# Optimization experiments

Measured on AMD Instinct MI355X. Metric: run time of the kernel, lower is better.

## Reference

```python
import jax, jax.numpy as jnp
import numpy as np

V = 32000   # vocab / input_size
H = 1024    # hidden_size (== embedding dim)
L = 2       # num_layers
B = 64      # batch
T = 256     # seq_len


def setup_inputs() -> dict:
    key = jax.random.key(0)
    ks = jax.random.split(key, 8)
    s = float(1.0 / np.sqrt(H))  # pytorch default uniform bound for LSTM/Linear
    return {
        "inputs": jax.random.randint(ks[0], (B, T), 0, V),
        "embed_table": jax.random.normal(ks[1], (V, H), jnp.float32),
        "W_ih": jax.random.uniform(ks[2], (L, 4 * H, H), jnp.float32, -s, s),
        "W_hh": jax.random.uniform(ks[3], (L, 4 * H, H), jnp.float32, -s, s),
        "b_ih": jax.random.uniform(ks[4], (L, 4 * H), jnp.float32, -s, s),
        "b_hh": jax.random.uniform(ks[5], (L, 4 * H), jnp.float32, -s, s),
        "W_proj": jax.random.uniform(ks[6], (V, H), jnp.float32, -s, s),
        "b_proj": jnp.zeros((V,), jnp.float32),  # module fills bias with 0
    }


def _lstm_layer(x, Wih, Whh, bih, bhh):
    # x: [B, T, H]. Precompute input contribution for all steps (one big GEMM).
    xg = jnp.einsum("bth,gh->btg", x, Wih) + bih + bhh  # [B, T, 4H]
    h0 = jnp.zeros((x.shape[0], Whh.shape[1]), x.dtype)
    c0 = h0

    def step(carry, xt):
        h, c = carry
        gates = xt + h @ Whh.T  # [B, 4H]
        i, f, g, o = jnp.split(gates, 4, axis=-1)  # pytorch gate order i,f,g,o
        i = jax.nn.sigmoid(i)
        f = jax.nn.sigmoid(f)
        g = jnp.tanh(g)
        o = jax.nn.sigmoid(o)
        c = f * c + i * g
        h = o * jnp.tanh(c)
        return (h, c), h

    (hT, cT), ys = jax.lax.scan(step, (h0, c0), jnp.swapaxes(xg, 0, 1))
    return jnp.swapaxes(ys, 0, 1), hT, cT  # [B,T,H], [B,H], [B,H]


def reference(inputs, embed_table, W_ih, W_hh, b_ih, b_hh, W_proj, b_proj):
    x = embed_table[inputs]  # [B, T, H]
    h_n, c_n = [], []
    for l in range(L):  # small fixed layer loop
        x, hT, cT = _lstm_layer(x, W_ih[l], W_hh[l], b_ih[l], b_hh[l])
        h_n.append(hT)
        c_n.append(cT)
    last_output = x[:, -1]                      # squeeze(output[:, -1]) with B>1 -> [B, H]
    logits = last_output @ W_proj.T + b_proj    # [B, V]
    return last_output, logits, jnp.stack(h_n), jnp.stack(c_n)
```

## Files before the change

### kernel.cpp

```cpp
#include <hip/hip_runtime.h>
#include <hip/hip_bf16.h>
#include <stdint.h>
#include <stddef.h>

typedef __hip_bfloat16 bf16;
typedef __attribute__((ext_vector_type(8))) short bfrag;
typedef __attribute__((ext_vector_type(4))) float ffrag;
typedef unsigned long long u64;

#define HDIM 1024
#define BATCH 64
#define TSTEPS 256
#define GDIM 4096
#define VOCAB 32000

#define HSLOT 16384ull

__device__ __forceinline__ bf16 f2b(float x) { return __float2bfloat16(x); }
__device__ __forceinline__ short f2bs(float x) {
  bf16 b = __float2bfloat16(x);
  return *reinterpret_cast<short*>(&b);
}
__device__ __forceinline__ float bs2f(unsigned short u) {
  union { unsigned int i; float f; } v;
  v.i = ((unsigned int)u) << 16;
  return v.f;
}
__device__ __forceinline__ ffrag mfma16(bfrag a, bfrag b, ffrag c) {
  return __builtin_amdgcn_mfma_f32_16x16x32_bf16(a, b, c, 0, 0, 0);
}
__device__ __forceinline__ float sigm(float x) { return 1.0f / (1.0f + __expf(-x)); }
__device__ __forceinline__ float tanhfast(float x) {
  float e = __expf(2.0f * x);
  return 1.0f - 2.0f / (e + 1.0f);
}

__device__ __forceinline__ void store_u16_agent(unsigned short* p, unsigned short v) {
  __hip_atomic_store(p, v, __ATOMIC_RELAXED, __HIP_MEMORY_SCOPE_AGENT);
}
__device__ __forceinline__ unsigned load_u32_agent(const unsigned* p) {
  return __hip_atomic_load(p, __ATOMIC_RELAXED, __HIP_MEMORY_SCOPE_AGENT);
}
__device__ __forceinline__ void store_u32_agent(unsigned* p, unsigned v) {
  __hip_atomic_store(p, v, __ATOMIC_RELAXED, __HIP_MEMORY_SCOPE_AGENT);
}

__global__ void convert_bf16_kernel(const float* __restrict__ src, bf16* __restrict__ dst, int n4) {
  int i = blockIdx.x * 256 + threadIdx.x;
  if (i >= n4) return;
  float4 v = reinterpret_cast<const float4*>(src)[i];
  ushort4 o;
  o.x = (unsigned short)f2bs(v.x);
  o.y = (unsigned short)f2bs(v.y);
  o.z = (unsigned short)f2bs(v.z);
  o.w = (unsigned short)f2bs(v.w);
  reinterpret_cast<ushort4*>(dst)[i] = o;
}

__global__ void embed_kernel(const int* __restrict__ ids, const float* __restrict__ table,
                             bf16* __restrict__ x, int n4) {
  int i = blockIdx.x * 256 + threadIdx.x;
  if (i >= n4) return;
  int row = i >> 8;
  int c4 = i & 255;
  int tok = ids[row];
  float4 v = reinterpret_cast<const float4*>(table)[(size_t)tok * 256 + c4];
  ushort4 o;
  o.x = (unsigned short)f2bs(v.x);
  o.y = (unsigned short)f2bs(v.y);
  o.z = (unsigned short)f2bs(v.z);
  o.w = (unsigned short)f2bs(v.w);
  reinterpret_cast<ushort4*>(x)[i] = o;
}

#define BMX 128
#define BNX 128
#define BKX 64

template<int LYR>
__launch_bounds__(256, 2)
__global__ void gemm_xg_kernel(const bf16* __restrict__ A,
                               const bf16* __restrict__ W,
                               const float* __restrict__ bih,
                               const float* __restrict__ bhh,
                               bf16* __restrict__ xg) {
  __shared__ bf16 As[BMX][BKX + 8];
  __shared__ bf16 Bs[BNX][BKX + 8];
  const int n0 = blockIdx.x * BNX;
  const int m0 = blockIdx.y * BMX;
  const int tid = threadIdx.x;
  const int w = tid >> 6, l = tid & 63;
  const int wm = (w >> 1) * 64, wn = (w & 1) * 64;
  const int lr = l & 15, lk = (l >> 4) * 8;

  ffrag acc[4][4];
#pragma unroll
  for (int i = 0; i < 4; ++i)
#pragma unroll
    for (int j = 0; j < 4; ++j) acc[i][j] = ffrag{0.f, 0.f, 0.f, 0.f};

  const int sr = tid >> 1, sh = (tid & 1) * 32;
  for (int kb = 0; kb < HDIM; kb += BKX) {
    __syncthreads();
    {
      if (LYR == 0) {
        const uint4* ga = reinterpret_cast<const uint4*>(&A[(size_t)(m0 + sr) * HDIM + kb + sh]);
        uint4* la = reinterpret_cast<uint4*>(&As[sr][sh]);
        la[0] = ga[0]; la[1] = ga[1]; la[2] = ga[2]; la[3] = ga[3];
      } else {
        const u64* hb = (const u64*)A;
        const int m = m0 + sr;
        const size_t tb = (size_t)(255 - (m >> 6)) * HSLOT + (m & 63);
        const int kg0 = (kb + sh) >> 3;
#pragma unroll
        for (int ii = 0; ii < 4; ++ii) {
          u64 lo = hb[tb + (size_t)(kg0 + ii) * 64];
          u64 hi = hb[tb + 8192 + (size_t)(kg0 + ii) * 64];
          *(u64*)&As[sr][sh + ii * 8]     = lo;
          *(u64*)&As[sr][sh + ii * 8 + 4] = hi;
        }
      }
      const uint4* gb = reinterpret_cast<const uint4*>(&W[(size_t)(n0 + sr) * HDIM + kb + sh]);
      uint4* lb = reinterpret_cast<uint4*>(&Bs[sr][sh]);
      lb[0] = gb[0]; lb[1] = gb[1]; lb[2] = gb[2]; lb[3] = gb[3];
    }
    __syncthreads();
#pragma unroll
    for (int ks = 0; ks < 2; ++ks) {
      const int ko = ks * 32 + lk;
      bfrag af[4], bfv[4];
#pragma unroll
      for (int i = 0; i < 4; ++i)
        af[i] = *reinterpret_cast<const bfrag*>(&As[wm + i * 16 + lr][ko]);
#pragma unroll
      for (int j = 0; j < 4; ++j)
        bfv[j] = *reinterpret_cast<const bfrag*>(&Bs[wn + j * 16 + lr][ko]);
#pragma unroll
      for (int i = 0; i < 4; ++i)
#pragma unroll
        for (int j = 0; j < 4; ++j)
          acc[i][j] = mfma16(af[i], bfv[j], acc[i][j]);
    }
  }
  const int rg = (l >> 4) * 4;
#pragma unroll
  for (int j = 0; j < 4; ++j) {
    const int n = n0 + wn + j * 16 + lr;
    const float bias = bih[n] + bhh[n];
    const int q = n >> 10, g = (n & 1023) >> 3, jj = n & 7;
    bf16* base = xg + (size_t)(q * 128 + g) * 16384 * 8 + jj;
#pragma unroll
    for (int i = 0; i < 4; ++i) {
#pragma unroll
      for (int r = 0; r < 4; ++r) {
        const int m = m0 + wm + i * 16 + rg + r;
        base[(size_t)m * 8] = f2b(acc[i][j][r] + bias);
      }
    }
  }
}

__launch_bounds__(256, 1)
__global__ void lstm_seq_kernel(const bf16* __restrict__ xg,
                                const bf16* __restrict__ Whh,
                                bf16* hist,
                                float* __restrict__ out_h,
                                float* __restrict__ out_c,
                                float* __restrict__ out_last,
                                unsigned* __restrict__ flags,
                                int xbs, int xts) {
  __shared__ float gxp[2][16][65];
  const int id = blockIdx.x;
  const int bg = id & 3, cg16 = id >> 2;
  const int tid = threadIdx.x;
  const int w = tid >> 6, l = tid & 63;
  const int lr = l & 15, lkg = l >> 4;
  const int kh = w >> 1, ch = w & 1;
  const int q = lr >> 2, jn = lr & 3;

  bfrag breg0[16], breg1[16];
  {
    const int colbase = cg16 * 16 + ch * 8;
    const size_t r0 = ((size_t)q * HDIM + colbase + jn) * HDIM + kh * 512 + lkg * 8;
    const size_t r1 = ((size_t)q * HDIM + colbase + 4 + jn) * HDIM + kh * 512 + lkg * 8;
#pragma unroll
    for (int ks = 0; ks < 16; ++ks) {
      breg0[ks] = *reinterpret_cast<const bfrag*>(&Whh[r0 + ks * 32]);
      breg1[ks] = *reinterpret_cast<const bfrag*>(&Whh[r1 + ks * 32]);
    }
  }

  const int eb = tid & 15, cl = tid >> 4;
  const int b_glob = bg * 16 + eb;
  const int gpl = cg16 * 2 + (cl >> 3);
  const int xjj = cl & 7;
  const int shalf = (cl >> 2) & 1, sjj = cl & 3;
  float c = 0.0f;

  u64* hb = (u64*)hist;
  const size_t arow = (size_t)(kh * 64 + lkg) * 64 + bg * 16 + lr;
  const unsigned* fv = flags + bg * 64;
  const unsigned short* xgu = (const unsigned short*)xg;

  unsigned short xn[4];
#pragma unroll
  for (int qq = 0; qq < 4; ++qq)
    xn[qq] = xgu[(((size_t)qq * 128 + gpl) * 16384 + (size_t)b_glob * xbs) * 8 + xjj];

#pragma unroll 1
  for (int t = 0; t < TSTEPS; ++t) {
    if (t > 0) {
      const unsigned tt = (unsigned)t;
      for (;;) {
        unsigned f = load_u32_agent(&fv[l]);
        if (__all((int)(f >= tt))) break;
        __builtin_amdgcn_s_sleep(1);
      }
    }
    __builtin_amdgcn_sched_barrier(0);
    asm volatile("" ::: "memory");

    const u64* hin = hb + (size_t)(TSTEPS - t) * HSLOT;
    ffrag a0 = ffrag{0.f, 0.f, 0.f, 0.f};
    ffrag a1 = ffrag{0.f, 0.f, 0.f, 0.f};
#pragma unroll
    for (int ks = 0; ks < 16; ++ks) {
      union { u64 u[2]; bfrag f; } au;
      au.u[0] = hin[arow + ks * 256];
      au.u[1] = hin[8192 + arow + ks * 256];
      a0 = mfma16(au.f, breg0[ks], a0);
      a1 = mfma16(au.f, breg1[ks], a1);
    }
    {
      const int cb = ch * 8;
#pragma unroll
      for (int r = 0; r < 4; ++r) {
        gxp[kh][lkg * 4 + r][q * 16 + cb + jn]     = a0[r];
        gxp[kh][lkg * 4 + r][q * 16 + cb + 4 + jn] = a1[r];
      }
    }
    __syncthreads();

    const float gi = gxp[0][eb][cl]      + gxp[1][eb][cl]      + bs2f(xn[0]);
    const float gf = gxp[0][eb][16 + cl] + gxp[1][eb][16 + cl] + bs2f(xn[1]);
    const float gg = gxp[0][eb][32 + cl] + gxp[1][eb][32 + cl] + bs2f(xn[2]);
    const float go = gxp[0][eb][48 + cl] + gxp[1][eb][48 + cl] + bs2f(xn[3]);
    c = sigm(gf) * c + sigm(gi) * tanhfast(gg);
    const float h = sigm(go) * tanhfast(c);

    u64* hout = hb + (size_t)(255 - t) * HSLOT;
    store_u16_agent((unsigned short*)(hout + (size_t)shalf * 8192 + gpl * 64 + b_glob) + sjj,
                    (unsigned short)f2bs(h));
    if (t == TSTEPS - 1) {
      const int col = cg16 * 16 + cl;
      out_h[(size_t)b_glob * HDIM + col] = h;
      out_c[(size_t)b_glob * HDIM + col] = c;
      if (out_last) out_last[(size_t)b_glob * HDIM + col] = h;
    }
    __builtin_amdgcn_s_waitcnt(0);
    __syncthreads();
    if (t < TSTEPS - 1) {
      if (tid == 0) store_u32_agent(&flags[bg * 64 + cg16], (unsigned)(t + 1));
#pragma unroll
      for (int qq = 0; qq < 4; ++qq)
        xn[qq] = xgu[(((size_t)qq * 128 + gpl) * 16384 +
                      (size_t)b_glob * xbs + (size_t)(t + 1) * xts) * 8 + xjj];
    }
    __builtin_amdgcn_sched_barrier(0);
  }
}

__launch_bounds__(256, 2)
__global__ void logits_kernel(const bf16* __restrict__ hfin,
                              const float* __restrict__ Wp,
                              const float* __restrict__ bp,
                              float* __restrict__ out) {
  const int tid = threadIdx.x;
  const int w = tid >> 6, l = tid & 63;
  const int lr = l & 15, lkg = l >> 4, lk = lkg * 8;
  const int col = blockIdx.x * 64 + w * 16 + lr;
  const float* wrow = &Wp[(size_t)col * HDIM];
  const u64* hb = (const u64*)hfin;
  ffrag acc[4];
#pragma unroll
  for (int i = 0; i < 4; ++i) acc[i] = ffrag{0.f, 0.f, 0.f, 0.f};
#pragma unroll 2
  for (int ks = 0; ks < 32; ++ks) {
    const int k = ks * 32 + lk;
    float4 wa = *reinterpret_cast<const float4*>(&wrow[k]);
    float4 wb = *reinterpret_cast<const float4*>(&wrow[k + 4]);
    bfrag bv;
    bv[0] = f2bs(wa.x); bv[1] = f2bs(wa.y); bv[2] = f2bs(wa.z); bv[3] = f2bs(wa.w);
    bv[4] = f2bs(wb.x); bv[5] = f2bs(wb.y); bv[6] = f2bs(wb.z); bv[7] = f2bs(wb.w);
    const size_t kg = (size_t)(ks * 4 + lkg);
#pragma unroll
    for (int i = 0; i < 4; ++i) {
      union { u64 u[2]; bfrag f; } av;
      av.u[0] = hb[kg * 64 + i * 16 + lr];
      av.u[1] = hb[8192 + kg * 64 + i * 16 + lr];
      acc[i] = mfma16(av.f, bv, acc[i]);
    }
  }
  const float bias = bp[col];
#pragma unroll
  for (int i = 0; i < 4; ++i) {
#pragma unroll
    for (int r = 0; r < 4; ++r) {
      const int b = i * 16 + (l >> 4) * 4 + r;
      out[(size_t)b * VOCAB + col] = acc[i][r] + bias;
    }
  }
}

extern "C" void kernel_launch(void* const* d_in, const int* in_sizes, int n_in,
                              void* d_out, int out_size, void* d_ws, size_t ws_size,
                              hipStream_t stream) {
  const int*   ids   = (const int*)d_in[0];
  const float* table = (const float*)d_in[1];
  const float* Wih   = (const float*)d_in[2];
  const float* Whh   = (const float*)d_in[3];
  const float* bih   = (const float*)d_in[4];
  const float* bhh   = (const float*)d_in[5];
  const float* Wp    = (const float*)d_in[6];
  const float* bp    = (const float*)d_in[7];
  float* out = (float*)d_out;

  char* ws = (char*)d_ws;
  const size_t HISTB_SZ = 257ull * 131072ull;
  const size_t OFF_XG  = 0;
  const size_t OFF_HA  = OFF_XG + (size_t)512 * 16384 * 8 * 2;
  const size_t OFF_HB  = OFF_HA + HISTB_SZ;
  const size_t OFF_WIH = OFF_HB + HISTB_SZ;
  const size_t OFF_WHH = OFF_WIH + (size_t)2 * GDIM * HDIM * 2;
  const size_t OFF_SYNC= OFF_WHH + (size_t)2 * GDIM * HDIM * 2;

  bf16* xg    = (bf16*)(ws + OFF_XG);
  bf16* xb    = (bf16*)(ws + OFF_HA);
  bf16* histA = (bf16*)(ws + OFF_HA);
  bf16* histB = (bf16*)(ws + OFF_HB);
  bf16* wihb  = (bf16*)(ws + OFF_WIH);
  bf16* whhb  = (bf16*)(ws + OFF_WHH);
  unsigned* sync = (unsigned*)(ws + OFF_SYNC);

  (void)hipMemsetAsync(sync, 0, 16384, stream);
  (void)hipMemsetAsync(ws + OFF_HA + 33554432ull, 0, 131072, stream);
  (void)hipMemsetAsync(ws + OFF_HB + 33554432ull, 0, 131072, stream);

  const int nconv4 = 2 * GDIM * HDIM / 4;
  convert_bf16_kernel<<<nconv4 / 256, 256, 0, stream>>>(Wih, wihb, nconv4);
  convert_bf16_kernel<<<nconv4 / 256, 256, 0, stream>>>(Whh, whhb, nconv4);
  const int nemb4 = BATCH * TSTEPS * HDIM / 4;
  embed_kernel<<<nemb4 / 256, 256, 0, stream>>>(ids, table, xb, nemb4);

  float* out_last   = out;
  float* out_logits = out + 65536;
  float* out_hn     = out + 2113536;
  float* out_cn     = out + 2244608;

  gemm_xg_kernel<0><<<dim3(GDIM / BNX, (BATCH * TSTEPS) / BMX), 256, 0, stream>>>(
      xb, wihb, bih, bhh, xg);
  lstm_seq_kernel<<<256, 256, 0, stream>>>(
      xg, whhb, histA, out_hn, out_cn, nullptr, sync, 256, 1);

  gemm_xg_kernel<1><<<dim3(GDIM / BNX, (BATCH * TSTEPS) / BMX), 256, 0, stream>>>(
      histA, wihb + (size_t)GDIM * HDIM, bih + GDIM, bhh + GDIM, xg);
  lstm_seq_kernel<<<256, 256, 0, stream>>>(
      xg, whhb + (size_t)GDIM * HDIM, histB,
      out_hn + (size_t)BATCH * HDIM, out_cn + (size_t)BATCH * HDIM,
      out_last, sync + 256, 1, 64);

  logits_kernel<<<VOCAB / 64, 256, 0, stream>>>(histB, Wp, bp, out_logits);
}
```

Measured before the change: 2.175 ms.

## Overlap layer-2 input GEMM with layer-1 recurrence via flag-gated fused blocks

Layer 1's recurrent kernel is launched with 4096 extra blocks that compute layer 2's input-projection GEMM. Each GEMM tile spin-waits on the layer-1 step flags until its two timesteps of hidden state exist, then computes that tile. The layer-0 GEMM now reads embeddings in time-major order, so the gate buffer is time-major for both layers. Flag polling is also done by one wave followed by a block barrier. The aim is to hide the separate layer-2 GEMM launch behind the serial recurrence. The risks are that spinning GEMM blocks contend with the latency-critical recurrent blocks, and that correctness depends on the recurrent blocks being co-resident.

New measurement: 3.743 ms. +72.1%, slower.

```diff
diff --git a/kernel.cpp b/kernel.cpp
--- a/kernel.cpp
+++ b/kernel.cpp
@@ -73,21 +73,16 @@
   reinterpret_cast<ushort4*>(x)[i] = o;
 }
 
-#define BMX 128
-#define BNX 128
-#define BKX 64
-
-template<int LYR>
 __launch_bounds__(256, 2)
-__global__ void gemm_xg_kernel(const bf16* __restrict__ A,
-                               const bf16* __restrict__ W,
-                               const float* __restrict__ bih,
-                               const float* __restrict__ bhh,
-                               bf16* __restrict__ xg) {
-  __shared__ bf16 As[BMX][BKX + 8];
-  __shared__ bf16 Bs[BNX][BKX + 8];
-  const int n0 = blockIdx.x * BNX;
-  const int m0 = blockIdx.y * BMX;
+__global__ void gemm_xg0_kernel(const bf16* __restrict__ A,
+                                const bf16* __restrict__ W,
+                                const float* __restrict__ bih,
+                                const float* __restrict__ bhh,
+                                bf16* __restrict__ xg) {
+  __shared__ bf16 As[128][72];
+  __shared__ bf16 Bs[128][72];
+  const int n0 = blockIdx.x * 128;
+  const int m0 = blockIdx.y * 128;
   const int tid = threadIdx.x;
   const int w = tid >> 6, l = tid & 63;
   const int wm = (w >> 1) * 64, wn = (w & 1) * 64;
@@ -100,26 +95,14 @@
     for (int j = 0; j < 4; ++j) acc[i][j] = ffrag{0.f, 0.f, 0.f, 0.f};
 
   const int sr = tid >> 1, sh = (tid & 1) * 32;
-  for (int kb = 0; kb < HDIM; kb += BKX) {
+  for (int kb = 0; kb < HDIM; kb += 64) {
     __syncthreads();
     {
-      if (LYR == 0) {
-        const uint4* ga = reinterpret_cast<const uint4*>(&A[(size_t)(m0 + sr) * HDIM + kb + sh]);
-        uint4* la = reinterpret_cast<uint4*>(&As[sr][sh]);
-        la[0] = ga[0]; la[1] = ga[1]; la[2] = ga[2]; la[3] = ga[3];
-      } else {
-        const u64* hb = (const u64*)A;
-        const int m = m0 + sr;
-        const size_t tb = (size_t)(255 - (m >> 6)) * HSLOT + (m & 63);
-        const int kg0 = (kb + sh) >> 3;
-#pragma unroll
-        for (int ii = 0; ii < 4; ++ii) {
-          u64 lo = hb[tb + (size_t)(kg0 + ii) * 64];
-          u64 hi = hb[tb + 8192 + (size_t)(kg0 + ii) * 64];
-          *(u64*)&As[sr][sh + ii * 8]     = lo;
-          *(u64*)&As[sr][sh + ii * 8 + 4] = hi;
-        }
-      }
+      const int m = m0 + sr;
+      const int bb = m & 63, tt = m >> 6;
+      const uint4* ga = reinterpret_cast<const uint4*>(&A[((size_t)bb * 256 + tt) * HDIM + kb + sh]);
+      uint4* la = reinterpret_cast<uint4*>(&As[sr][sh]);
+      la[0] = ga[0]; la[1] = ga[1]; la[2] = ga[2]; la[3] = ga[3];
       const uint4* gb = reinterpret_cast<const uint4*>(&W[(size_t)(n0 + sr) * HDIM + kb + sh]);
       uint4* lb = reinterpret_cast<uint4*>(&Bs[sr][sh]);
       lb[0] = gb[0]; lb[1] = gb[1]; lb[2] = gb[2]; lb[3] = gb[3];
@@ -155,6 +138,206 @@
       for (int r = 0; r < 4; ++r) {
         const int m = m0 + wm + i * 16 + rg + r;
         base[(size_t)m * 8] = f2b(acc[i][j][r] + bias);
+      }
+    }
+  }
+}
+
+__launch_bounds__(256, 2)
+__global__ void lstm1_fused_kernel(bf16* __restrict__ xg,
+                                   const bf16* __restrict__ whh1,
+                                   const bf16* __restrict__ wih2,
+                                   const float* __restrict__ bih2,
+                                   const float* __restrict__ bhh2,
+                                   bf16* hist,
+                                   float* __restrict__ out_h,
+                                   float* __restrict__ out_c,
+                                   unsigned* __restrict__ fL1) {
+  __shared__ __align__(16) char smraw[36864];
+  const int id = blockIdx.x;
+  const int tid = threadIdx.x;
+  const int w = tid >> 6, l = tid & 63;
+
+  if (id < 256) {
+    float (*gxp)[16][65] = (float(*)[16][65])smraw;
+    const int bg = id & 3, cg16 = id >> 2;
+    const int lr = l & 15, lkg = l >> 4;
+    const int kh = w >> 1, ch = w & 1;
+    const int q = lr >> 2, jn = lr & 3;
+
+    bfrag breg0[16], breg1[16];
+    {
+      const int colbase = cg16 * 16 + ch * 8;
+      const size_t r0 = ((size_t)q * HDIM + colbase + jn) * HDIM + kh * 512 + lkg * 8;
+      const size_t r1 = ((size_t)q * HDIM + colbase + 4 + jn) * HDIM + kh * 512 + lkg * 8;
+#pragma unroll
+      for (int ks = 0; ks < 16; ++ks) {
+        breg0[ks] = *reinterpret_cast<const bfrag*>(&whh1[r0 + ks * 32]);
+        breg1[ks] = *reinterpret_cast<const bfrag*>(&whh1[r1 + ks * 32]);
+      }
+    }
+
+    const int eb = tid & 15, cl = tid >> 4;
+    const int b_glob = bg * 16 + eb;
+    const int gpl = cg16 * 2 + (cl >> 3);
+    const int xjj = cl & 7;
+    const int shalf = (cl >> 2) & 1, sjj = cl & 3;
+    float c = 0.0f;
+
+    u64* hb = (u64*)hist;
+    const size_t arow = (size_t)(kh * 64 + lkg) * 64 + bg * 16 + lr;
+    const unsigned* fv = fL1 + bg * 64;
+    const unsigned short* xgu = (const unsigned short*)xg;
+
+    unsigned short xn[4];
+#pragma unroll
+    for (int qq = 0; qq < 4; ++qq)
+      xn[qq] = xgu[(((size_t)qq * 128 + gpl) * 16384 + (size_t)b_glob) * 8 + xjj];
+
+#pragma unroll 1
+    for (int t = 0; t < TSTEPS; ++t) {
+      if (t > 0) {
+        if (w == 0) {
+          const unsigned tt = (unsigned)t;
+          for (;;) {
+            unsigned f = load_u32_agent(&fv[l]);
+            if (__all((int)(f >= tt))) break;
+            __builtin_amdgcn_s_sleep(2);
+          }
+        }
+        __syncthreads();
+      }
+      __builtin_amdgcn_sched_barrier(0);
+      asm volatile("" ::: "memory");
+
+      const u64* hin = hb + (size_t)(TSTEPS - t) * HSLOT;
+      ffrag a0 = ffrag{0.f, 0.f, 0.f, 0.f};
+      ffrag a1 = ffrag{0.f, 0.f, 0.f, 0.f};
+#pragma unroll
+      for (int ks = 0; ks < 16; ++ks) {
+        union { u64 u[2]; bfrag f; } au;
+        au.u[0] = hin[arow + ks * 256];
+        au.u[1] = hin[8192 + arow + ks * 256];
+        a0 = mfma16(au.f, breg0[ks], a0);
+        a1 = mfma16(au.f, breg1[ks], a1);
+      }
+      {
+        const int cb = ch * 8;
+#pragma unroll
+        for (int r = 0; r < 4; ++r) {
+          gxp[kh][lkg * 4 + r][q * 16 + cb + jn]     = a0[r];
+          gxp[kh][lkg * 4 + r][q * 16 + cb + 4 + jn] = a1[r];
+        }
+      }
+      __syncthreads();
+
+      const float gi = gxp[0][eb][cl]      + gxp[1][eb][cl]      + bs2f(xn[0]);
+      const float gf = gxp[0][eb][16 + cl] + gxp[1][eb][16 + cl] + bs2f(xn[1]);
+      const float gg = gxp[0][eb][32 + cl] + gxp[1][eb][32 + cl] + bs2f(xn[2]);
+      const float go = gxp[0][eb][48 + cl] + gxp[1][eb][48 + cl] + bs2f(xn[3]);
+      c = sigm(gf) * c + sigm(gi) * tanhfast(gg);
+      const float h = sigm(go) * tanhfast(c);
+
+      u64* hout = hb + (size_t)(255 - t) * HSLOT;
+      store_u16_agent((unsigned short*)(hout + (size_t)shalf * 8192 + gpl * 64 + b_glob) + sjj,
+                      (unsigned short)f2bs(h));
+      if (t == TSTEPS - 1) {
+        const int col = cg16 * 16 + cl;
+        out_h[(size_t)b_glob * HDIM + col] = h;
+        out_c[(size_t)b_glob * HDIM + col] = c;
+      } else {
+#pragma unroll
+        for (int qq = 0; qq < 4; ++qq)
+          xn[qq] = xgu[(((size_t)qq * 128 + gpl) * 16384 +
+                        (size_t)(t + 1) * 64 + b_glob) * 8 + xjj];
+      }
+      __builtin_amdgcn_s_waitcnt(0);
+      __syncthreads();
+      if (tid == 0) store_u32_agent(&fL1[bg * 64 + cg16], (unsigned)(t + 1));
+      __builtin_amdgcn_sched_barrier(0);
+    }
+  } else {
+    bf16 (*As)[72] = (bf16(*)[72])smraw;
+    bf16 (*Bs)[72] = (bf16(*)[72])(smraw + 18432);
+    const int gid = id - 256;
+    const int my = gid >> 5, nx = gid & 31;
+    const int m0 = my * 128, n0 = nx * 128;
+
+    if (w == 0) {
+      const unsigned target = (unsigned)(my * 2 + 2);
+      for (;;) {
+        unsigned f0 = load_u32_agent(&fL1[l]);
+        unsigned f1 = load_u32_agent(&fL1[64 + l]);
+        unsigned f2 = load_u32_agent(&fL1[128 + l]);
+        unsigned f3 = load_u32_agent(&fL1[192 + l]);
+        int ok = (f0 >= target) && (f1 >= target) && (f2 >= target) && (f3 >= target);
+        if (__all(ok)) break;
+        __builtin_amdgcn_s_sleep(32);
+      }
+    }
+    __syncthreads();
+    __builtin_amdgcn_sched_barrier(0);
+    asm volatile("" ::: "memory");
+
+    const int wm = (w >> 1) * 64, wn = (w & 1) * 64;
+    const int lr = l & 15, lk = (l >> 4) * 8;
+    ffrag acc[4][4];
+#pragma unroll
+    for (int i = 0; i < 4; ++i)
+#pragma unroll
+      for (int j = 0; j < 4; ++j) acc[i][j] = ffrag{0.f, 0.f, 0.f, 0.f};
+
+    const int sr = tid >> 1, sh = (tid & 1) * 32;
+    const u64* hbA = (const u64*)hist;
+    for (int kb = 0; kb < HDIM; kb += 64) {
+      __syncthreads();
+      {
+        const int m = m0 + sr;
+        const size_t tb = (size_t)(255 - (m >> 6)) * HSLOT + (m & 63);
+        const int kg0 = (kb + sh) >> 3;
+#pragma unroll
+        for (int ii = 0; ii < 4; ++ii) {
+          u64 lo = hbA[tb + (size_t)(kg0 + ii) * 64];
+          u64 hi = hbA[tb + 8192 + (size_t)(kg0 + ii) * 64];
+          *(u64*)&As[sr][sh + ii * 8]     = lo;
+          *(u64*)&As[sr][sh + ii * 8 + 4] = hi;
+        }
+        const uint4* gb = reinterpret_cast<const uint4*>(&wih2[(size_t)(n0 + sr) * HDIM + kb + sh]);
+        uint4* lb = reinterpret_cast<uint4*>(&Bs[sr][sh]);
+        lb[0] = gb[0]; lb[1] = gb[1]; lb[2] = gb[2]; lb[3] = gb[3];
+      }
+      __syncthreads();
+#pragma unroll
+      for (int ks = 0; ks < 2; ++ks) {
+        const int ko = ks * 32 + lk;
+        bfrag af[4], bfv[4];
+#pragma unroll
+        for (int i = 0; i < 4; ++i)
+          af[i] = *reinterpret_cast<const bfrag*>(&As[wm + i * 16 + lr][ko]);
+#pragma unroll
+        for (int j = 0; j < 4; ++j)
+          bfv[j] = *reinterpret_cast<const bfrag*>(&Bs[wn + j * 16 + lr][ko]);
+#pragma unroll
+        for (int i = 0; i < 4; ++i)
+#pragma unroll
+          for (int j = 0; j < 4; ++j)
+            acc[i][j] = mfma16(af[i], bfv[j], acc[i][j]);
+      }
+    }
+    const int rg = (l >> 4) * 4;
+#pragma unroll
+    for (int j = 0; j < 4; ++j) {
+      const int n = n0 + wn + j * 16 + lr;
+      const float bias = bih2[n] + bhh2[n];
+      const int q = n >> 10, g = (n & 1023) >> 3, jj = n & 7;
+      bf16* base = xg + (size_t)(q * 128 + g) * 16384 * 8 + jj;
+#pragma unroll
+      for (int i = 0; i < 4; ++i) {
+#pragma unroll
+        for (int r = 0; r < 4; ++r) {
+          const int m = m0 + wm + i * 16 + rg + r;
+          base[(size_t)m * 8] = f2b(acc[i][j][r] + bias);
+        }
       }
     }
   }
@@ -167,8 +350,7 @@
                                 float* __restrict__ out_h,
                                 float* __restrict__ out_c,
                                 float* __restrict__ out_last,
-                                unsigned* __restrict__ flags,
-                                int xbs, int xts) {
+                                unsigned* __restrict__ flags) {
   __shared__ float gxp[2][16][65];
   const int id = blockIdx.x;
   const int bg = id & 3, cg16 = id >> 2;
@@ -205,17 +387,20 @@
   unsigned short xn[4];
 #pragma unroll
   for (int qq = 0; qq < 4; ++qq)
-    xn[qq] = xgu[(((size_t)qq * 128 + gpl) * 16384 + (size_t)b_glob * xbs) * 8 + xjj];
+    xn[qq] = xgu[(((size_t)qq * 128 + gpl) * 16384 + (size_t)b_glob) * 8 + xjj];
 
 #pragma unroll 1
   for (int t = 0; t < TSTEPS; ++t) {
     if (t > 0) {
-      const unsigned tt = (unsigned)t;
-      for (;;) {
-        unsigned f = load_u32_agent(&fv[l]);
-        if (__all((int)(f >= tt))) break;
-        __builtin_amdgcn_s_sleep(1);
-      }
+      if (w == 0) {
+        const unsigned tt = (unsigned)t;
+        for (;;) {
+          unsigned f = load_u32_agent(&fv[l]);
+          if (__all((int)(f >= tt))) break;
+          __builtin_amdgcn_s_sleep(2);
+        }
+      }
+      __syncthreads();
     }
     __builtin_amdgcn_sched_barrier(0);
     asm volatile("" ::: "memory");
@@ -256,16 +441,16 @@
       out_h[(size_t)b_glob * HDIM + col] = h;
       out_c[(size_t)b_glob * HDIM + col] = c;
       if (out_last) out_last[(size_t)b_glob * HDIM + col] = h;
+    } else {
+#pragma unroll
+      for (int qq = 0; qq < 4; ++qq)
+        xn[qq] = xgu[(((size_t)qq * 128 + gpl) * 16384 +
+                      (size_t)(t + 1) * 64 + b_glob) * 8 + xjj];
     }
     __builtin_amdgcn_s_waitcnt(0);
     __syncthreads();
-    if (t < TSTEPS - 1) {
-      if (tid == 0) store_u32_agent(&flags[bg * 64 + cg16], (unsigned)(t + 1));
-#pragma unroll
-      for (int qq = 0; qq < 4; ++qq)
-        xn[qq] = xgu[(((size_t)qq * 128 + gpl) * 16384 +
-                      (size_t)b_glob * xbs + (size_t)(t + 1) * xts) * 8 + xjj];
-    }
+    if (t < TSTEPS - 1 && tid == 0)
+      store_u32_agent(&flags[bg * 64 + cg16], (unsigned)(t + 1));
     __builtin_amdgcn_sched_barrier(0);
   }
 }
@@ -341,6 +526,8 @@
   bf16* wihb  = (bf16*)(ws + OFF_WIH);
   bf16* whhb  = (bf16*)(ws + OFF_WHH);
   unsigned* sync = (unsigned*)(ws + OFF_SYNC);
+  unsigned* fL1 = sync;
+  unsigned* fL2 = sync + 256;
 
   (void)hipMemsetAsync(sync, 0, 16384, stream);
   (void)hipMemsetAsync(ws + OFF_HA + 33554432ull, 0, 131072, stream);
@@ -357,17 +544,16 @@
   float* out_hn     = out + 2113536;
   float* out_cn     = out + 2244608;
 
-  gemm_xg_kernel<0><<<dim3(GDIM / BNX, (BATCH * TSTEPS) / BMX), 256, 0, stream>>>(
-      xb, wihb, bih, bhh, xg);
-  lstm_seq_kernel<<<256, 256, 0, stream>>>(
-      xg, whhb, histA, out_hn, out_cn, nullptr, sync, 256, 1);
-
-  gemm_xg_kernel<1><<<dim3(GDIM / BNX, (BATCH * TSTEPS) / BMX), 256, 0, stream>>>(
-      histA, wihb + (size_t)GDIM * HDIM, bih + GDIM, bhh + GDIM, xg);
+  gemm_xg0_kernel<<<dim3(32, 128), 256, 0, stream>>>(xb, wihb, bih, bhh, xg);
+
+  lstm1_fused_kernel<<<256 + 4096, 256, 0, stream>>>(
+      xg, whhb, wihb + (size_t)GDIM * HDIM, bih + GDIM, bhh + GDIM,
+      histA, out_hn, out_cn, fL1);
+
   lstm_seq_kernel<<<256, 256, 0, stream>>>(
       xg, whhb + (size_t)GDIM * HDIM, histB,
       out_hn + (size_t)BATCH * HDIM, out_cn + (size_t)BATCH * HDIM,
-      out_last, sync + 256, 1, 64);
+      out_last, fL2);
 
   logits_kernel<<<VOCAB / 64, 256, 0, stream>>>(histB, Wp, bp, out_logits);
 }
```
